# Kernel optimization log

Measured on AMD Instinct MI355X. Metric: run time of the kernel, lower is better.

## Reference

```python
import jax, jax.numpy as jnp
import numpy as np

B, S, H = 4, 2048, 768
NUM_HEADS = 12
HEAD_DIM = H // NUM_HEADS


def setup_inputs() -> dict:
    key = jax.random.key(0)
    k1, k2, k3 = jax.random.split(key, 3)
    hidden_states = jax.random.normal(k1, (B, S, H), dtype=jnp.float32)
    # torch Linear weight [out,in]; store transposed [in,out] for x @ W
    w_qkv = jax.random.normal(k2, (H, 3 * H), dtype=jnp.float32) * (1.0 / np.sqrt(H))
    w_out = jax.random.normal(k3, (H, H), dtype=jnp.float32) * (1.0 / np.sqrt(H))
    return {"hidden_states": hidden_states, "w_qkv": w_qkv, "w_out": w_out}


def reference(hidden_states, w_qkv, w_out):
    b, s, h = hidden_states.shape
    qkv = hidden_states @ w_qkv                      # [b,s,3h]
    qkv = qkv.reshape(b, s, 3, NUM_HEADS, HEAD_DIM)
    qkv = jnp.transpose(qkv, (2, 0, 3, 1, 4))        # [3,b,nh,s,hd]
    q, k, v = qkv[0], qkv[1], qkv[2]
    scale = 1.0 / np.sqrt(HEAD_DIM).astype(np.float32)
    scores = jnp.einsum('bhqd,bhkd->bhqk', q, k) * scale   # [b,nh,s,s]
    causal = jnp.triu(jnp.ones((s, s), dtype=bool), k=1)
    scores = jnp.where(causal, jnp.float32(-jnp.inf), scores)
    attn = jax.nn.softmax(scores, axis=-1)
    # dropout is identity in eval mode
    out = jnp.einsum('bhqk,bhkd->bhqd', attn, v)      # [b,nh,s,hd]
    out = jnp.transpose(out, (0, 2, 1, 3)).reshape(b, s, h)
    return out @ w_out
```

## Files before the change

kernel.cpp:

```cpp
#include <hip/hip_runtime.h>
#include <stdint.h>

#define B_ 4
#define S_ 2048
#define H_ 768
#define NH_ 12
#define HD_ 64
#define BH_ (B_ * NH_)

#define QSCALE 0.18033688011112042f
#define MFIX 8.0f

typedef __attribute__((ext_vector_type(4))) float f32x4;
typedef __attribute__((ext_vector_type(8))) __bf16 bf16x8;
typedef __attribute__((ext_vector_type(8))) unsigned short ushort8;

__device__ __forceinline__ unsigned short bf16rne(float f) {
  union { float f; unsigned int u; } v;
  v.f = f;
  unsigned int u = v.u;
  return (unsigned short)((u + 0x7fffu + ((u >> 16) & 1u)) >> 16);
}

#if __has_builtin(__builtin_amdgcn_cvt_pk_bf16_f32)
__device__ __forceinline__ unsigned int pk2(float a, float b) {
  auto r = __builtin_amdgcn_cvt_pk_bf16_f32(a, b);
  return *(unsigned int*)&r;
}
#else
__device__ __forceinline__ unsigned int pk2(float a, float b) {
  return (unsigned int)bf16rne(a) | ((unsigned int)bf16rne(b) << 16);
}
#endif

#if __has_builtin(__builtin_amdgcn_exp2f)
#define EXP2F(x) __builtin_amdgcn_exp2f(x)
#else
#define EXP2F(x) exp2f(x)
#endif

__device__ __forceinline__ void gll16(const void* g, void* l) {
  __builtin_amdgcn_global_load_lds(
      (const __attribute__((address_space(1))) unsigned int*)g,
      (__attribute__((address_space(3))) unsigned int*)l, 16, 0, 0);
}

__device__ __forceinline__ void tconv_body(const float* __restrict__ in,
                                           unsigned short* __restrict__ out,
                                           int R, int C, int bx, int by,
                                           unsigned short (*tile)[72], int tid) {
  int c0 = bx * 64, r0 = by * 64;
#pragma unroll
  for (int i = 0; i < 4; ++i) {
    int c = i * 256 + tid;
    int row = c >> 4, col4 = (c & 15) * 4;
    float4 v = *(const float4*)(in + (size_t)(r0 + row) * C + c0 + col4);
    *(uint2*)(&tile[row][col4]) = (uint2){pk2(v.x, v.y), pk2(v.z, v.w)};
  }
  __syncthreads();
#pragma unroll
  for (int i = 0; i < 2; ++i) {
    int c = i * 256 + tid;
    int oc = c >> 3, r8 = (c & 7) * 8;
    ushort8 v;
#pragma unroll
    for (int j = 0; j < 8; ++j) v[j] = tile[r8 + j][oc];
    *(ushort8*)(out + (size_t)(c0 + oc) * R + r0 + r8) = v;
  }
}

__global__ __launch_bounds__(256) void prep_kernel(const float* __restrict__ hs,
                                                   const float* __restrict__ wqkv,
                                                   const float* __restrict__ wout,
                                                   unsigned short* __restrict__ Xbf,
                                                   unsigned short* __restrict__ Wqkvt,
                                                   unsigned short* __restrict__ Woutt) {
  __shared__ unsigned short tile[64][72];
  int bid = blockIdx.x, tid = threadIdx.x;
  if (bid < 3072) {
    int i = (bid * 256 + tid) * 8;
    const float4* p = (const float4*)(hs + i);
    float4 a = p[0], b = p[1];
    uint4 r = {pk2(a.x, a.y), pk2(a.z, a.w), pk2(b.x, b.y), pk2(b.z, b.w)};
    *(uint4*)(Xbf + i) = r;
  } else if (bid < 3504) {
    int idx = bid - 3072;
    tconv_body(wqkv, Wqkvt, 768, 2304, idx % 36, idx / 36, tile, tid);
  } else {
    int idx = bid - 3504;
    tconv_body(wout, Woutt, 768, 768, idx % 12, idx / 12, tile, tid);
  }
}

template <int MODE>
__device__ __forceinline__ void gemm_core(const unsigned short* __restrict__ A,
                                          const unsigned short* __restrict__ Bm,
                                          void* __restrict__ Cout, int N, int K,
                                          int bm, int bn,
                                          unsigned short* As, unsigned short* Bs) {
  int tid = threadIdx.x;
  int lane = tid & 63, wave = tid >> 6;
  int quad = lane >> 4, l16 = lane & 15;
  int wm = (wave & 1) * 64, wn = (wave >> 1) * 64;
  const unsigned short* Ag = A + (size_t)bm * 128 * K;
  const unsigned short* Bg = Bm + (size_t)bn * 128 * K;

  f32x4 zero = {0.f, 0.f, 0.f, 0.f};
  f32x4 acc[4][4];
#pragma unroll
  for (int mt = 0; mt < 4; ++mt)
#pragma unroll
    for (int nt = 0; nt < 4; ++nt) acc[mt][nt] = zero;

  for (int k0 = 0; k0 < K; k0 += 32) {
#pragma unroll
    for (int i = 0; i < 2; ++i) {
      int c = i * 256 + tid;
      int row = c >> 2, off = (c & 3) * 8;
      gll16(Ag + (size_t)row * K + k0 + off, As + c * 8);
      gll16(Bg + (size_t)row * K + k0 + off, Bs + c * 8);
    }
    __syncthreads();
    bf16x8 af[4], bf[4];
#pragma unroll
    for (int mt = 0; mt < 4; ++mt)
      af[mt] = *(const bf16x8*)(As + (wm + mt * 16 + l16) * 32 + quad * 8);
#pragma unroll
    for (int nt = 0; nt < 4; ++nt)
      bf[nt] = *(const bf16x8*)(Bs + (wn + nt * 16 + l16) * 32 + quad * 8);
#pragma unroll
    for (int mt = 0; mt < 4; ++mt)
#pragma unroll
      for (int nt = 0; nt < 4; ++nt) {
        if (MODE == 2)
          acc[mt][nt] = __builtin_amdgcn_mfma_f32_16x16x32_bf16(af[mt], bf[nt], acc[mt][nt], 0, 0, 0);
        else
          acc[mt][nt] = __builtin_amdgcn_mfma_f32_16x16x32_bf16(bf[nt], af[mt], acc[mt][nt], 0, 0, 0);
      }
    __syncthreads();
  }

  if (MODE == 0) {
    unsigned short* qkv = (unsigned short*)Cout;
    int which = (bn >= 6);
#pragma unroll
    for (int mt = 0; mt < 4; ++mt)
#pragma unroll
      for (int nt = 0; nt < 4; ++nt) {
        int f0 = bn * 128 + wn + nt * 16 + quad * 4;
        int tm = bm * 128 + wm + mt * 16 + l16;
        int rem = f0 - which * 768;
        int head = rem >> 6, d0 = rem & 63;
        int b = tm >> 11, s = tm & 2047;
        if (which == 0) {
          uint2 pkv = {pk2(acc[mt][nt][0] * QSCALE, acc[mt][nt][1] * QSCALE),
                       pk2(acc[mt][nt][2] * QSCALE, acc[mt][nt][3] * QSCALE)};
          *(uint2*)(qkv + (((size_t)b * NH_ + head) * S_ + s) * HD_ + d0) = pkv;
        } else {
          uint2 pkv = {pk2(acc[mt][nt][0], acc[mt][nt][1]),
                       pk2(acc[mt][nt][2], acc[mt][nt][3])};
          int dd0 = (((d0 >> 3) ^ (s & 7)) << 3) | (d0 & 7);
          *(uint2*)(qkv + (((size_t)(BH_ + b * NH_ + head)) * S_ + s) * HD_ + dd0) = pkv;
        }
      }
  } else if (MODE == 2) {
    unsigned short* vt = (unsigned short*)Cout;
#pragma unroll
    for (int mt = 0; mt < 4; ++mt)
#pragma unroll
      for (int nt = 0; nt < 4; ++nt) {
        int f = bn * 128 + wn + nt * 16 + l16;
        int t0 = bm * 128 + wm + mt * 16 + quad * 4;
        int rem = f - 1536;
        int head = rem >> 6, d = rem & 63;
        int b = t0 >> 11, s0 = t0 & 2047;
        int tile = s0 >> 6, sin = s0 & 63;
        int pos = (((sin >> 3) ^ (d & 7)) << 3) | (sin & 7);
        uint2 pkv = {pk2(acc[mt][nt][0], acc[mt][nt][1]),
                     pk2(acc[mt][nt][2], acc[mt][nt][3])};
        *(uint2*)(vt + (((size_t)(b * NH_ + head)) * HD_ + d) * S_ + tile * 64 + pos) = pkv;
      }
  } else {
    float* outp = (float*)Cout;
#pragma unroll
    for (int mt = 0; mt < 4; ++mt)
#pragma unroll
      for (int nt = 0; nt < 4; ++nt) {
        int f0 = bn * 128 + wn + nt * 16 + quad * 4;
        int tm = bm * 128 + wm + mt * 16 + l16;
        *(f32x4*)(outp + (size_t)tm * N + f0) = acc[mt][nt];
      }
  }
}

__global__ __launch_bounds__(256) void gemm_qkv(const unsigned short* __restrict__ A,
                                                const unsigned short* __restrict__ Bm,
                                                unsigned short* __restrict__ QK,
                                                unsigned short* __restrict__ Vt) {
  __shared__ unsigned short As[128 * 32];
  __shared__ unsigned short Bs[128 * 32];
  int bm = blockIdx.x, bn = blockIdx.y;
  if (bn < 12)
    gemm_core<0>(A, Bm, QK, 2304, 768, bm, bn, As, Bs);
  else
    gemm_core<2>(A, Bm, Vt, 2304, 768, bm, bn, As, Bs);
}

__global__ __launch_bounds__(256) void gemm_out(const unsigned short* __restrict__ A,
                                                const unsigned short* __restrict__ Bm,
                                                float* __restrict__ Cout) {
  __shared__ unsigned short As[128 * 32];
  __shared__ unsigned short Bs[128 * 32];
  gemm_core<1>(A, Bm, Cout, 768, 768, blockIdx.x, blockIdx.y, As, Bs);
}

__global__ __launch_bounds__(512, 6) void attn_kernel(const unsigned short* __restrict__ Q,
                                                      const unsigned short* __restrict__ Kg,
                                                      const unsigned short* __restrict__ Vt,
                                                      unsigned short* __restrict__ O) {
  __shared__ unsigned short Ks[2][64 * 64];
  __shared__ unsigned short Vs[2][64 * 64];
  __shared__ unsigned short Ps[8][16 * 64];
  const int pi_[16] = {0, 1, 3, 5, 7, 9, 11, 13, 15, 14, 12, 10, 8, 6, 4, 2};
  int bh = blockIdx.x;
  int y = blockIdx.y;
  int qt = pi_[(bh + y) & 15];
  int tid = threadIdx.x, lane = tid & 63, wave = tid >> 6;
  int quad = lane >> 4, l16 = lane & 15;
  const unsigned short* Qp = Q + (size_t)bh * S_ * HD_;
  const unsigned short* Kp = Kg + (size_t)bh * S_ * HD_;
  const unsigned short* Vp = Vt + (size_t)bh * HD_ * S_;
  int q0 = qt * 128;
  int qrow = q0 + wave * 16 + l16;
  int kmax_w = (q0 + wave * 16 + 15) >> 6;
  int kmax_b = 2 * qt + 1;

  auto stage = [&](int t, int buf) {
    int row = tid >> 3, off = (tid & 7) * 8;
    gll16(Kp + (size_t)t * 64 * HD_ + row * HD_ + off, &Ks[buf][tid * 8]);
    gll16(Vp + (size_t)row * S_ + t * 64 + off, &Vs[buf][tid * 8]);
  };

  stage(0, 0);

  bf16x8 qf[2];
#pragma unroll
  for (int ks = 0; ks < 2; ++ks)
    qf[ks] = *(const bf16x8*)(Qp + (size_t)qrow * HD_ + ks * 32 + quad * 8);

  bf16x8 ones;
#pragma unroll
  for (int j = 0; j < 8; ++j) ones[j] = (__bf16)1.0f;

  f32x4 zero = {0.f, 0.f, 0.f, 0.f};
  float l_i = 0.f;
  f32x4 o[4];
#pragma unroll
  for (int nt = 0; nt < 4; ++nt) o[nt] = zero;

  for (int t = 0; t <= kmax_b; ++t) {
    __syncthreads();
    if (t < kmax_b) stage(t + 1, (t + 1) & 1);
    if (t > kmax_w) continue;
    const unsigned short* Kb = Ks[t & 1];
    const unsigned short* Vb = Vs[t & 1];

    f32x4 sf[4];
#pragma unroll
    for (int nt = 0; nt < 4; ++nt) sf[nt] = zero;
#pragma unroll
    for (int ks = 0; ks < 2; ++ks)
#pragma unroll
      for (int nt = 0; nt < 4; ++nt) {
        bf16x8 kf = *(const bf16x8*)(Kb + (nt * 16 + l16) * 64 + (((ks * 4 + quad) ^ (l16 & 7)) << 3));
        sf[nt] = __builtin_amdgcn_mfma_f32_16x16x32_bf16(kf, qf[ks], sf[nt], 0, 0, 0);
      }

    if (t == kmax_w) {
#pragma unroll
      for (int nt = 0; nt < 4; ++nt)
#pragma unroll
        for (int r = 0; r < 4; ++r)
          if (t * 64 + nt * 16 + quad * 4 + r > qrow) sf[nt][r] = -1e30f;
    }

#pragma unroll
    for (int nt = 0; nt < 4; ++nt) {
      uint2 pkv = {pk2(EXP2F(sf[nt][0] - MFIX), EXP2F(sf[nt][1] - MFIX)),
                   pk2(EXP2F(sf[nt][2] - MFIX), EXP2F(sf[nt][3] - MFIX))};
      int kvblk = nt * 2 + (quad >> 1);
      *(uint2*)(&Ps[wave][l16 * 64 + (((kvblk ^ (l16 & 7)) << 3) | ((quad & 1) * 4))]) = pkv;
    }

    f32x4 rsv = zero;
#pragma unroll
    for (int ks = 0; ks < 2; ++ks) {
      bf16x8 pf = *(const bf16x8*)(&Ps[wave][l16 * 64 + (((ks * 4 + quad) ^ (l16 & 7)) << 3)]);
      rsv = __builtin_amdgcn_mfma_f32_16x16x32_bf16(ones, pf, rsv, 0, 0, 0);
#pragma unroll
      for (int nt = 0; nt < 4; ++nt) {
        bf16x8 vf = *(const bf16x8*)(Vb + (nt * 16 + l16) * 64 + (((ks * 4 + quad) ^ (l16 & 7)) << 3));
        o[nt] = __builtin_amdgcn_mfma_f32_16x16x32_bf16(vf, pf, o[nt], 0, 0, 0);
      }
    }
    l_i += rsv[0];
  }

  float inv = 1.f / l_i;
  int b = bh / NH_, h = bh % NH_;
#pragma unroll
  for (int nt = 0; nt < 4; ++nt) {
    uint2 pkv = {pk2(o[nt][0] * inv, o[nt][1] * inv),
                 pk2(o[nt][2] * inv, o[nt][3] * inv)};
    int d0 = nt * 16 + quad * 4;
    *(uint2*)(O + ((size_t)b * S_ + qrow) * H_ + h * HD_ + d0) = pkv;
  }
}

extern "C" void kernel_launch(void* const* d_in, const int* in_sizes, int n_in,
                              void* d_out, int out_size, void* d_ws, size_t ws_size,
                              hipStream_t stream) {
  (void)in_sizes; (void)n_in; (void)out_size; (void)ws_size;
  const float* hs = (const float*)d_in[0];
  const float* wqkv = (const float*)d_in[1];
  const float* wout = (const float*)d_in[2];
  float* out = (float*)d_out;

  unsigned short* Xbf = (unsigned short*)d_ws;
  unsigned short* Wqkvt = Xbf + (size_t)8192 * 768;
  unsigned short* Woutt = Wqkvt + (size_t)2304 * 768;
  unsigned short* QK = Woutt + (size_t)768 * 768;
  unsigned short* Vt = QK + (size_t)2 * BH_ * S_ * HD_;
  unsigned short* Attn = Xbf;

  prep_kernel<<<3648, 256, 0, stream>>>(hs, wqkv, wout, Xbf, Wqkvt, Woutt);
  gemm_qkv<<<dim3(64, 18), 256, 0, stream>>>(Xbf, Wqkvt, QK, Vt);
  attn_kernel<<<dim3(48, 16), 512, 0, stream>>>(QK, QK + (size_t)BH_ * S_ * HD_, Vt, Attn);
  gemm_out<<<dim3(64, 6), 256, 0, stream>>>(Attn, Woutt, out);
}
```

Baseline: 196.2 us.

## Switch attention to 32x32 MFMA with 4 waves; load GEMM B directly from global

The attention kernel moves from 8 waves of 16x16x32 MFMA to 4 waves each handling 32 query rows with 32x32x16 MFMA, so each K/V fragment read from LDS feeds more work. The ones-MFMA row sum is replaced by a per-lane scalar sum plus a cross-half shuffle, and the fixed max offset is removed. Both GEMMs stop staging B in LDS and read its fragments straight from global/L2, and they use a swizzled 1D block index for locality. The cost is higher register pressure from the 16-wide accumulators, uncoalesced global B reads, and a risk of exp overflow without the MFIX offset.

```diff
diff --git a/kernel.cpp b/kernel.cpp
--- a/kernel.cpp
+++ b/kernel.cpp
@@ -9,9 +9,9 @@
 #define BH_ (B_ * NH_)
 
 #define QSCALE 0.18033688011112042f
-#define MFIX 8.0f
 
 typedef __attribute__((ext_vector_type(4))) float f32x4;
+typedef __attribute__((ext_vector_type(16))) float f32x16;
 typedef __attribute__((ext_vector_type(8))) __bf16 bf16x8;
 typedef __attribute__((ext_vector_type(8))) unsigned short ushort8;
 
@@ -96,8 +96,7 @@
 __device__ __forceinline__ void gemm_core(const unsigned short* __restrict__ A,
                                           const unsigned short* __restrict__ Bm,
                                           void* __restrict__ Cout, int N, int K,
-                                          int bm, int bn,
-                                          unsigned short* As, unsigned short* Bs) {
+                                          int bm, int bn, unsigned short* As) {
   int tid = threadIdx.x;
   int lane = tid & 63, wave = tid >> 6;
   int quad = lane >> 4, l16 = lane & 15;
@@ -118,16 +117,15 @@
       int c = i * 256 + tid;
       int row = c >> 2, off = (c & 3) * 8;
       gll16(Ag + (size_t)row * K + k0 + off, As + c * 8);
-      gll16(Bg + (size_t)row * K + k0 + off, Bs + c * 8);
     }
     __syncthreads();
     bf16x8 af[4], bf[4];
 #pragma unroll
+    for (int nt = 0; nt < 4; ++nt)
+      bf[nt] = *(const bf16x8*)(Bg + (size_t)(wn + nt * 16 + l16) * K + k0 + quad * 8);
+#pragma unroll
     for (int mt = 0; mt < 4; ++mt)
       af[mt] = *(const bf16x8*)(As + (wm + mt * 16 + l16) * 32 + quad * 8);
-#pragma unroll
-    for (int nt = 0; nt < 4; ++nt)
-      bf[nt] = *(const bf16x8*)(Bs + (wn + nt * 16 + l16) * 32 + quad * 8);
 #pragma unroll
     for (int mt = 0; mt < 4; ++mt)
 #pragma unroll
@@ -198,65 +196,69 @@
                                                 unsigned short* __restrict__ QK,
                                                 unsigned short* __restrict__ Vt) {
   __shared__ unsigned short As[128 * 32];
-  __shared__ unsigned short Bs[128 * 32];
-  int bm = blockIdx.x, bn = blockIdx.y;
+  int id = blockIdx.x;
+  int bm = (id & 7) * 8 + ((id >> 3) & 7);
+  int bn = id >> 6;
   if (bn < 12)
-    gemm_core<0>(A, Bm, QK, 2304, 768, bm, bn, As, Bs);
+    gemm_core<0>(A, Bm, QK, 2304, 768, bm, bn, As);
   else
-    gemm_core<2>(A, Bm, Vt, 2304, 768, bm, bn, As, Bs);
+    gemm_core<2>(A, Bm, Vt, 2304, 768, bm, bn, As);
 }
 
 __global__ __launch_bounds__(256) void gemm_out(const unsigned short* __restrict__ A,
                                                 const unsigned short* __restrict__ Bm,
                                                 float* __restrict__ Cout) {
   __shared__ unsigned short As[128 * 32];
-  __shared__ unsigned short Bs[128 * 32];
-  gemm_core<1>(A, Bm, Cout, 768, 768, blockIdx.x, blockIdx.y, As, Bs);
-}
-
-__global__ __launch_bounds__(512, 6) void attn_kernel(const unsigned short* __restrict__ Q,
-                                                      const unsigned short* __restrict__ Kg,
-                                                      const unsigned short* __restrict__ Vt,
-                                                      unsigned short* __restrict__ O) {
+  int id = blockIdx.x;
+  int bm = (id & 7) * 8 + ((id >> 3) & 7);
+  int bn = id >> 6;
+  gemm_core<1>(A, Bm, Cout, 768, 768, bm, bn, As);
+}
+
+__global__ __launch_bounds__(256) void attn_kernel(const unsigned short* __restrict__ Q,
+                                                   const unsigned short* __restrict__ Kg,
+                                                   const unsigned short* __restrict__ Vt,
+                                                   unsigned short* __restrict__ O) {
   __shared__ unsigned short Ks[2][64 * 64];
   __shared__ unsigned short Vs[2][64 * 64];
-  __shared__ unsigned short Ps[8][16 * 64];
+  __shared__ unsigned short Ps[4][32 * 64];
   const int pi_[16] = {0, 1, 3, 5, 7, 9, 11, 13, 15, 14, 12, 10, 8, 6, 4, 2};
   int bh = blockIdx.x;
   int y = blockIdx.y;
   int qt = pi_[(bh + y) & 15];
   int tid = threadIdx.x, lane = tid & 63, wave = tid >> 6;
-  int quad = lane >> 4, l16 = lane & 15;
+  int l32 = lane & 31, lh = lane >> 5;
   const unsigned short* Qp = Q + (size_t)bh * S_ * HD_;
   const unsigned short* Kp = Kg + (size_t)bh * S_ * HD_;
   const unsigned short* Vp = Vt + (size_t)bh * HD_ * S_;
   int q0 = qt * 128;
-  int qrow = q0 + wave * 16 + l16;
-  int kmax_w = (q0 + wave * 16 + 15) >> 6;
+  int qcol = q0 + wave * 32 + l32;
+  int kmax_w = (q0 + wave * 32 + 31) >> 6;
   int kmax_b = 2 * qt + 1;
 
   auto stage = [&](int t, int buf) {
-    int row = tid >> 3, off = (tid & 7) * 8;
-    gll16(Kp + (size_t)t * 64 * HD_ + row * HD_ + off, &Ks[buf][tid * 8]);
-    gll16(Vp + (size_t)row * S_ + t * 64 + off, &Vs[buf][tid * 8]);
+#pragma unroll
+    for (int i = 0; i < 2; ++i) {
+      int c = i * 256 + tid;
+      int row = c >> 3, off = (c & 7) * 8;
+      gll16(Kp + (size_t)t * 64 * HD_ + row * HD_ + off, &Ks[buf][c * 8]);
+      gll16(Vp + (size_t)row * S_ + t * 64 + off, &Vs[buf][c * 8]);
+    }
   };
 
   stage(0, 0);
 
-  bf16x8 qf[2];
-#pragma unroll
-  for (int ks = 0; ks < 2; ++ks)
-    qf[ks] = *(const bf16x8*)(Qp + (size_t)qrow * HD_ + ks * 32 + quad * 8);
-
-  bf16x8 ones;
-#pragma unroll
-  for (int j = 0; j < 8; ++j) ones[j] = (__bf16)1.0f;
-
-  f32x4 zero = {0.f, 0.f, 0.f, 0.f};
-  float l_i = 0.f;
-  f32x4 o[4];
-#pragma unroll
-  for (int nt = 0; nt < 4; ++nt) o[nt] = zero;
+  bf16x8 qf[4];
+#pragma unroll
+  for (int st = 0; st < 4; ++st)
+    qf[st] = *(const bf16x8*)(Qp + (size_t)qcol * HD_ + st * 16 + lh * 8);
+
+  float l0 = 0.f, l1 = 0.f, l2 = 0.f, l3 = 0.f;
+  f32x16 o[2];
+#pragma unroll
+  for (int mb = 0; mb < 2; ++mb)
+#pragma unroll
+    for (int e = 0; e < 16; ++e) o[mb][e] = 0.f;
 
   for (int t = 0; t <= kmax_b; ++t) {
     __syncthreads();
@@ -265,56 +267,69 @@
     const unsigned short* Kb = Ks[t & 1];
     const unsigned short* Vb = Vs[t & 1];
 
-    f32x4 sf[4];
-#pragma unroll
-    for (int nt = 0; nt < 4; ++nt) sf[nt] = zero;
-#pragma unroll
-    for (int ks = 0; ks < 2; ++ks)
-#pragma unroll
-      for (int nt = 0; nt < 4; ++nt) {
-        bf16x8 kf = *(const bf16x8*)(Kb + (nt * 16 + l16) * 64 + (((ks * 4 + quad) ^ (l16 & 7)) << 3));
-        sf[nt] = __builtin_amdgcn_mfma_f32_16x16x32_bf16(kf, qf[ks], sf[nt], 0, 0, 0);
+    f32x16 sf[2];
+#pragma unroll
+    for (int mb = 0; mb < 2; ++mb)
+#pragma unroll
+      for (int e = 0; e < 16; ++e) sf[mb][e] = 0.f;
+#pragma unroll
+    for (int st = 0; st < 4; ++st)
+#pragma unroll
+      for (int mb = 0; mb < 2; ++mb) {
+        int row = mb * 32 + l32;
+        bf16x8 kf = *(const bf16x8*)(Kb + row * 64 + (((st * 2 + lh) ^ (row & 7)) << 3));
+        sf[mb] = __builtin_amdgcn_mfma_f32_32x32x16_bf16(kf, qf[st], sf[mb], 0, 0, 0);
       }
 
     if (t == kmax_w) {
 #pragma unroll
-      for (int nt = 0; nt < 4; ++nt)
-#pragma unroll
-        for (int r = 0; r < 4; ++r)
-          if (t * 64 + nt * 16 + quad * 4 + r > qrow) sf[nt][r] = -1e30f;
-    }
-
-#pragma unroll
-    for (int nt = 0; nt < 4; ++nt) {
-      uint2 pkv = {pk2(EXP2F(sf[nt][0] - MFIX), EXP2F(sf[nt][1] - MFIX)),
-                   pk2(EXP2F(sf[nt][2] - MFIX), EXP2F(sf[nt][3] - MFIX))};
-      int kvblk = nt * 2 + (quad >> 1);
-      *(uint2*)(&Ps[wave][l16 * 64 + (((kvblk ^ (l16 & 7)) << 3) | ((quad & 1) * 4))]) = pkv;
-    }
-
-    f32x4 rsv = zero;
-#pragma unroll
-    for (int ks = 0; ks < 2; ++ks) {
-      bf16x8 pf = *(const bf16x8*)(&Ps[wave][l16 * 64 + (((ks * 4 + quad) ^ (l16 & 7)) << 3)]);
-      rsv = __builtin_amdgcn_mfma_f32_16x16x32_bf16(ones, pf, rsv, 0, 0, 0);
-#pragma unroll
-      for (int nt = 0; nt < 4; ++nt) {
-        bf16x8 vf = *(const bf16x8*)(Vb + (nt * 16 + l16) * 64 + (((ks * 4 + quad) ^ (l16 & 7)) << 3));
-        o[nt] = __builtin_amdgcn_mfma_f32_16x16x32_bf16(vf, pf, o[nt], 0, 0, 0);
-      }
-    }
-    l_i += rsv[0];
-  }
-
+      for (int mb = 0; mb < 2; ++mb)
+#pragma unroll
+        for (int e = 0; e < 16; ++e) {
+          int kv = t * 64 + mb * 32 + (e & 3) + 8 * (e >> 2) + 4 * lh;
+          if (kv > qcol) sf[mb][e] = -1e30f;
+        }
+    }
+
+#pragma unroll
+    for (int mb = 0; mb < 2; ++mb)
+#pragma unroll
+      for (int g = 0; g < 4; ++g) {
+        float e0 = EXP2F(sf[mb][g * 4 + 0]);
+        float e1 = EXP2F(sf[mb][g * 4 + 1]);
+        float e2 = EXP2F(sf[mb][g * 4 + 2]);
+        float e3 = EXP2F(sf[mb][g * 4 + 3]);
+        l0 += e0; l1 += e1; l2 += e2; l3 += e3;
+        uint2 pkv = {pk2(e0, e1), pk2(e2, e3)};
+        int blk = mb * 4 + g;
+        *(uint2*)(&Ps[wave][l32 * 64 + ((((blk ^ (l32 & 7)) << 3)) | (lh * 4))]) = pkv;
+      }
+
+#pragma unroll
+    for (int st = 0; st < 4; ++st) {
+      bf16x8 pf = *(const bf16x8*)(&Ps[wave][l32 * 64 + (((st * 2 + lh) ^ (l32 & 7)) << 3)]);
+#pragma unroll
+      for (int mb = 0; mb < 2; ++mb) {
+        int row = mb * 32 + l32;
+        bf16x8 vf = *(const bf16x8*)(Vb + row * 64 + (((st * 2 + lh) ^ (row & 7)) << 3));
+        o[mb] = __builtin_amdgcn_mfma_f32_32x32x16_bf16(vf, pf, o[mb], 0, 0, 0);
+      }
+    }
+  }
+
+  float l_i = (l0 + l1) + (l2 + l3);
+  l_i += __shfl_xor(l_i, 32);
   float inv = 1.f / l_i;
   int b = bh / NH_, h = bh % NH_;
 #pragma unroll
-  for (int nt = 0; nt < 4; ++nt) {
-    uint2 pkv = {pk2(o[nt][0] * inv, o[nt][1] * inv),
-                 pk2(o[nt][2] * inv, o[nt][3] * inv)};
-    int d0 = nt * 16 + quad * 4;
-    *(uint2*)(O + ((size_t)b * S_ + qrow) * H_ + h * HD_ + d0) = pkv;
-  }
+  for (int mb = 0; mb < 2; ++mb)
+#pragma unroll
+    for (int g = 0; g < 4; ++g) {
+      uint2 pkv = {pk2(o[mb][g * 4 + 0] * inv, o[mb][g * 4 + 1] * inv),
+                   pk2(o[mb][g * 4 + 2] * inv, o[mb][g * 4 + 3] * inv)};
+      int d0 = mb * 32 + g * 8 + lh * 4;
+      *(uint2*)(O + ((size_t)b * S_ + qcol) * H_ + h * HD_ + d0) = pkv;
+    }
 }
 
 extern "C" void kernel_launch(void* const* d_in, const int* in_sizes, int n_in,
@@ -334,7 +349,7 @@
   unsigned short* Attn = Xbf;
 
   prep_kernel<<<3648, 256, 0, stream>>>(hs, wqkv, wout, Xbf, Wqkvt, Woutt);
-  gemm_qkv<<<dim3(64, 18), 256, 0, stream>>>(Xbf, Wqkvt, QK, Vt);
-  attn_kernel<<<dim3(48, 16), 512, 0, stream>>>(QK, QK + (size_t)BH_ * S_ * HD_, Vt, Attn);
-  gemm_out<<<dim3(64, 6), 256, 0, stream>>>(Attn, Woutt, out);
-}
+  gemm_qkv<<<1152, 256, 0, stream>>>(Xbf, Wqkvt, QK, Vt);
+  attn_kernel<<<dim3(48, 16), 256, 0, stream>>>(QK, QK + (size_t)BH_ * S_ * HD_, Vt, Attn);
+  gemm_out<<<384, 256, 0, stream>>>(Attn, Woutt, out);
+}
```

Result: slower. 273.8 us (+39.6%).
